# Performance work log

Hardware: AMD Instinct MI355X
Metric: run time of the kernel (lower is better)

Reference implementation:

```python
import jax, jax.numpy as jnp
import numpy as np

DIM = 96          # adapter bottleneck dim
K = 3             # conv kernel size

def quick_gelu(x):
    return x * jax.nn.sigmoid(1.702 * x)

def setup_inputs() -> dict:
    key = jax.random.key(0)
    ks = jax.random.split(key, 12)
    B, H, W, C = 64, 28, 28, 384
    x   = jax.random.normal(ks[0], (B, H, W, C), jnp.float32)
    # adapter down/up (xavier-ish scale for down; up is zero-init in the
    # original but we use small random so gradients flow in tests)
    Wd  = jax.random.normal(ks[1], (C, DIM), jnp.float32) * 0.05
    bd  = jnp.zeros((DIM,), jnp.float32)
    Wu  = jax.random.normal(ks[2], (DIM, C), jnp.float32) * 0.02
    bu  = jnp.zeros((C,), jnp.float32)
    # meta_net: Linear(C,64) -> ReLU -> Linear(64,64)
    Wm1 = jax.random.normal(ks[3], (C, 64), jnp.float32) * 0.05
    bm1 = jnp.zeros((64,), jnp.float32)
    Wm2 = jax.random.normal(ks[4], (64, 64), jnp.float32) * 0.1
    bm2 = jnp.zeros((64,), jnp.float32)
    # conv hypernet: Linear(64, DIM*DIM*K*K)
    Wh  = jax.random.normal(ks[5], (64, DIM * DIM * K * K), jnp.float32) * 0.01
    bh  = jnp.zeros((DIM * DIM * K * K,), jnp.float32)
    # learned layer embedding
    emb = jax.random.normal(ks[6], (64,), jnp.float32)
    return {"x": x, "Wd": Wd, "bd": bd, "Wm1": Wm1, "bm1": bm1,
            "Wm2": Wm2, "bm2": bm2, "Wh": Wh, "bh": bh, "emb": emb,
            "Wu": Wu, "bu": bu}

def reference(x, Wd, bd, Wm1, bm1, Wm2, bm2, Wh, bh, emb, Wu, bu):
    B, H, W, C = x.shape
    # meta_net(x) then mean over spatial dims -> per-sample prompt feature [B,64]
    h = jax.nn.relu(jnp.einsum('bhwc,cd->bhwd', x, Wm1) + bm1)
    prompt = jnp.mean(jnp.einsum('bhwd,de->bhwe', h, Wm2) + bm2, axis=(1, 2))  # [B,64]
    # hypernet: per-sample dynamic conv weights (fuse_type='add')
    wflat = (emb[None, :] + prompt) @ Wh + bh                 # [B, DIM*DIM*9]
    wconv = wflat.reshape(B * DIM, DIM, K, K)                 # grouped OIHW
    # adapter down + QuickGELU
    xd = quick_gelu(jnp.einsum('bhwc,cd->bhwd', x, Wd) + bd)  # [B,H,W,DIM]
    # fused batched dynamic conv via grouped conv (groups = B)
    xg = xd.transpose(0, 3, 1, 2).reshape(1, B * DIM, H, W)   # [1,B*DIM,H,W]
    yg = jax.lax.conv_general_dilated(
        xg, wconv, window_strides=(1, 1), padding=((1, 1), (1, 1)),
        dimension_numbers=('NCHW', 'OIHW', 'NCHW'), feature_group_count=B)
    y = yg.reshape(B, DIM, H, W).transpose(0, 2, 3, 1)        # [B,H,W,DIM]
    y = quick_gelu(y)  # dropout is identity in eval mode
    return jnp.einsum('bhwd,dc->bhwc', y, Wu) + bu
```

## Files before the change

kernel.cpp:

```cpp
#include <hip/hip_runtime.h>
#include <hip/hip_fp16.h>

#define BATCH 64
#define HH    28
#define WW2   28
#define HWPX  784
#define PTOT  50176
#define CIN   384
#define DIM   96
#define MDIM  64
#define JTOT  82944
#define WSAMP 82944

#define XD_OFF 0u
#define Y_OFF  9633792u
#define WP_OFF 19267584u
#define HS_OFF 29884416u
#define Z_OFF  29900800u
#define WUT_OFF 29917184u

typedef _Float16 f16x8 __attribute__((ext_vector_type(8)));
typedef _Float16 f16x4 __attribute__((ext_vector_type(4)));
typedef float f32x4 __attribute__((ext_vector_type(4)));

__device__ __forceinline__ float qgelu(float v) {
    return v / (1.f + __expf(-1.702f * v));
}

__global__ void k0_wcvt(const float* __restrict__ Wm1,
                        const float* __restrict__ Wd,
                        const float* __restrict__ Wu,
                        _Float16* __restrict__ Wt,
                        _Float16* __restrict__ WuT)
{
    int i = blockIdx.x * 256 + threadIdx.x;
    if (i < 61440) {
        int o = i / CIN, k = i - o * CIN;
        float v = (o < MDIM) ? Wm1[k * MDIM + o] : Wd[k * DIM + (o - MDIM)];
        Wt[i] = (_Float16)v;
    } else {
        int j = i - 61440;
        int c = j / DIM, d = j - c * DIM;
        WuT[j] = (_Float16)Wu[d * CIN + c];
    }
}

__global__ __launch_bounds__(512, 4) void k1_mfma(
    const float* __restrict__ x, const _Float16* __restrict__ Wt,
    const float* __restrict__ bm1, const float* __restrict__ bd,
    float* __restrict__ hsum, __half* __restrict__ xd)
{
    __shared__ char smem[25088];
    _Float16* xds = (_Float16*)smem;
    float*   hred = (float*)(smem + 24576);

    const int t = threadIdx.x;
    const int p0 = blockIdx.x * 128;
    const int lane = t & 63, w = t >> 6;
    const int wm = w >> 1, wn = w & 1;
    const int rl = lane & 15, q = lane >> 4;

    const float* a0 = x + (size_t)(p0 + wm * 32 + rl) * CIN + q * 8;
    const float* a1 = a0 + 16 * CIN;
    const _Float16* bp0 = Wt + (wn * 80 + rl) * CIN + q * 8;

    f32x4 acc[2][5];
    #pragma unroll
    for (int mf = 0; mf < 2; ++mf)
        #pragma unroll
        for (int nf = 0; nf < 5; ++nf) acc[mf][nf] = (f32x4){0.f, 0.f, 0.f, 0.f};

    #pragma unroll
    for (int kc = 0; kc < 12; ++kc) {
        f16x8 bv[5];
        #pragma unroll
        for (int nf = 0; nf < 5; ++nf)
            bv[nf] = *(const f16x8*)(bp0 + nf * 16 * CIN + kc * 32);

        float4 fa0 = *(const float4*)(a0 + kc * 32);
        float4 fa1 = *(const float4*)(a0 + kc * 32 + 4);
        float4 fb0 = *(const float4*)(a1 + kc * 32);
        float4 fb1 = *(const float4*)(a1 + kc * 32 + 4);

        f16x8 av[2];
        av[0][0] = (_Float16)fa0.x; av[0][1] = (_Float16)fa0.y;
        av[0][2] = (_Float16)fa0.z; av[0][3] = (_Float16)fa0.w;
        av[0][4] = (_Float16)fa1.x; av[0][5] = (_Float16)fa1.y;
        av[0][6] = (_Float16)fa1.z; av[0][7] = (_Float16)fa1.w;
        av[1][0] = (_Float16)fb0.x; av[1][1] = (_Float16)fb0.y;
        av[1][2] = (_Float16)fb0.z; av[1][3] = (_Float16)fb0.w;
        av[1][4] = (_Float16)fb1.x; av[1][5] = (_Float16)fb1.y;
        av[1][6] = (_Float16)fb1.z; av[1][7] = (_Float16)fb1.w;

        #pragma unroll
        for (int mf = 0; mf < 2; ++mf)
            #pragma unroll
            for (int nf = 0; nf < 5; ++nf)
                acc[mf][nf] = __builtin_amdgcn_mfma_f32_16x16x32_f16(
                    av[mf], bv[nf], acc[mf][nf], 0, 0, 0);
    }

    if (t < 128) hred[t] = 0.f;
    __syncthreads();

    const int s0 = p0 / HWPX, s_last = (p0 + 127) / HWPX;
    #pragma unroll
    for (int mf = 0; mf < 2; ++mf) {
        #pragma unroll
        for (int nf = 0; nf < 5; ++nf) {
            const int col = wn * 80 + nf * 16 + rl;
            #pragma unroll
            for (int j = 0; j < 4; ++j) {
                const int rr = wm * 32 + mf * 16 + q * 4 + j;
                float v = acc[mf][nf][j];
                if (col < 64) {
                    v = fmaxf(v + bm1[col], 0.f);
                    int sloc = (p0 + rr) / HWPX - s0;
                    atomicAdd(&hred[sloc * 64 + col], v);
                } else {
                    int e = col - 64;
                    xds[rr * 96 + e] = (_Float16)qgelu(v + bd[e]);
                }
            }
        }
    }
    __syncthreads();

    if (t < 128) {
        int sloc = t >> 6, col = t & 63, s = s0 + sloc;
        if (s <= s_last) atomicAdd(&hsum[s * 64 + col], hred[t]);
    }
    #pragma unroll
    for (int i = 0; i < 3; ++i) {
        int e = t + i * 512;
        *(uint4*)((__half*)xd + (size_t)p0 * 96 + e * 8) = *(uint4*)(xds + e * 8);
    }
}

__global__ void k2a_prompt(const float* __restrict__ hsum,
                           const float* __restrict__ Wm2,
                           const float* __restrict__ bm2,
                           const float* __restrict__ emb,
                           float* __restrict__ z)
{
    int idx = blockIdx.x * 256 + threadIdx.x;
    int b = idx >> 6, m = idx & 63;
    float acc = 0.f;
    #pragma unroll 8
    for (int d = 0; d < 64; ++d) acc += hsum[b * 64 + d] * Wm2[d * 64 + m];
    z[idx] = emb[m] + acc * (1.f / 784.f) + bm2[m];
}

__global__ __launch_bounds__(256) void k2b_hyper(
    const float* __restrict__ z, const float* __restrict__ Wh,
    const float* __restrict__ bh, __half* __restrict__ wperm)
{
    __shared__ float zs[4096];
    const int t = threadIdx.x;
    for (int idx = t; idx < 4096; idx += 256) zs[idx] = z[idx];
    const int j = blockIdx.x * 256 + t;
    float wh[64];
    #pragma unroll 8
    for (int m = 0; m < 64; ++m) wh[m] = Wh[(size_t)m * JTOT + j];
    __syncthreads();

    const int o = j / 864, rem = j % 864;
    const int i = rem / 9, t9 = rem % 9;
    const int base = o * 864 + t9 * 96 + i;
    const float bj = bh[j];
    for (int b = 0; b < 64; ++b) {
        float a = bj;
        const float4* zz = (const float4*)(zs + b * 64);
        #pragma unroll
        for (int m4 = 0; m4 < 16; ++m4) {
            float4 v = zz[m4];
            a += v.x * wh[4 * m4] + v.y * wh[4 * m4 + 1] +
                 v.z * wh[4 * m4 + 2] + v.w * wh[4 * m4 + 3];
        }
        wperm[(size_t)b * WSAMP + base] = __float2half(a);
    }
}

__global__ __launch_bounds__(256) void k3_mfma(
    const __half* __restrict__ xd, const __half* __restrict__ wperm,
    __half* __restrict__ y)
{
    __shared__ __half sm[17600];
    const int t = threadIdx.x;

    const int n = blockIdx.x;
    const int xcd = n & 7, jj0 = n >> 3;
    const int b = xcd * 8 + jj0 / 7;
    const int rt = jj0 % 7;
    const int h0 = rt * 4;

    if (t < 16) *(uint4*)(sm + 17472 + t * 8) = uint4{0u, 0u, 0u, 0u};
    for (int idx = t; idx < 2016; idx += 256) {
        int pix = idx / 12, q = idx - pix * 12;
        int r = pix / 28, col = pix - r * 28;
        int g = h0 - 1 + r;
        uint4 v = {0u, 0u, 0u, 0u};
        if ((unsigned)g < 28u)
            v = *(const uint4*)(xd + (size_t)(b * HWPX + g * 28 + col) * 96 + q * 8);
        *(uint4*)(sm + pix * 104 + q * 8) = v;
    }
    __syncthreads();

    const int lane = t & 63, w = t >> 6;
    const int wm = w >> 1, wn = w & 1;
    const int mloc = lane & 15, klo = (lane >> 4) * 8;
    const int base_m = wm * 64;

    int oh_[4], ow_[4]; bool pv[4];
    #pragma unroll
    for (int mf = 0; mf < 4; ++mf) {
        int p = base_m + mf * 16 + mloc;
        pv[mf] = (p < 112);
        int pp = pv[mf] ? p : 0;
        oh_[mf] = pp / 28; ow_[mf] = pp - oh_[mf] * 28;
    }
    const __half* wp = wperm + (size_t)b * WSAMP + (wn * 48 + mloc) * 864 + klo;

    f32x4 acc[4][3];
    #pragma unroll
    for (int mf = 0; mf < 4; ++mf)
        #pragma unroll
        for (int nf = 0; nf < 3; ++nf) acc[mf][nf] = (f32x4){0.f, 0.f, 0.f, 0.f};

    #pragma unroll
    for (int kh = 0; kh < 3; ++kh) {
        #pragma unroll
        for (int kw = 0; kw < 3; ++kw) {
            const int t9 = kh * 3 + kw;
            int abase[4];
            #pragma unroll
            for (int mf = 0; mf < 4; ++mf) {
                int iw = ow_[mf] + kw - 1;
                bool valid = pv[mf] && ((unsigned)iw < 28u);
                abase[mf] = valid ? ((oh_[mf] + kh) * 28 + iw) * 104 + klo
                                  : 17472 + klo;
            }
            #pragma unroll
            for (int ic = 0; ic < 3; ++ic) {
                f16x8 av[4], bv[3];
                #pragma unroll
                for (int nf = 0; nf < 3; ++nf)
                    bv[nf] = *(const f16x8*)(wp + nf * 13824 + t9 * 96 + ic * 32);
                #pragma unroll
                for (int mf = 0; mf < 4; ++mf)
                    av[mf] = *(const f16x8*)(sm + abase[mf] + ic * 32);
                #pragma unroll
                for (int mf = 0; mf < 4; ++mf)
                    #pragma unroll
                    for (int nf = 0; nf < 3; ++nf)
                        acc[mf][nf] = __builtin_amdgcn_mfma_f32_16x16x32_f16(
                            av[mf], bv[nf], acc[mf][nf], 0, 0, 0);
            }
        }
    }
    __syncthreads();

    #pragma unroll
    for (int mf = 0; mf < 4; ++mf) {
        #pragma unroll
        for (int nf = 0; nf < 3; ++nf) {
            const int o = wn * 48 + nf * 16 + mloc;
            #pragma unroll
            for (int j = 0; j < 4; ++j) {
                int p = base_m + mf * 16 + (lane >> 4) * 4 + j;
                if (p < 112)
                    sm[p * 104 + o] = __float2half(qgelu(acc[mf][nf][j]));
            }
        }
    }
    __syncthreads();
    for (int idx = t; idx < 1344; idx += 256) {
        int pix = idx / 12, q = idx - pix * 12;
        *(uint4*)(y + (size_t)(b * HWPX + h0 * 28 + pix) * 96 + q * 8) =
            *(uint4*)(sm + pix * 104 + q * 8);
    }
}

__global__ __launch_bounds__(512, 2) void k4_mfma(
    const __half* __restrict__ y, const _Float16* __restrict__ WuT,
    const float* __restrict__ bu, float* __restrict__ out)
{
    __shared__ __half ys[128 * 104];
    const int t = threadIdx.x;
    const int p0 = blockIdx.x * 128;

    #pragma unroll
    for (int i = 0; i < 3; ++i) {
        int idx = t + i * 512;
        int pix = idx / 12, q = idx - pix * 12;
        *(uint4*)(ys + pix * 104 + q * 8) =
            *(const uint4*)(y + (size_t)(p0 + pix) * 96 + q * 8);
    }

    const int lane = t & 63, w = t >> 6;
    const int wm = w >> 2, wn = w & 3;
    const int mloc = lane & 15, klo = (lane >> 4) * 8;

    float bcol[6];
    #pragma unroll
    for (int nf = 0; nf < 6; ++nf) bcol[nf] = bu[wn * 96 + nf * 16 + mloc];
    __syncthreads();

    f32x4 acc[4][6];
    #pragma unroll
    for (int mf = 0; mf < 4; ++mf)
        #pragma unroll
        for (int nf = 0; nf < 6; ++nf) acc[mf][nf] = (f32x4){0.f, 0.f, 0.f, 0.f};

    #pragma unroll
    for (int kc = 0; kc < 3; ++kc) {
        f16x8 av[4], bv[6];
        #pragma unroll
        for (int nf = 0; nf < 6; ++nf)
            bv[nf] = *(const f16x8*)(WuT + (wn * 96 + nf * 16 + mloc) * 96 + kc * 32 + klo);
        #pragma unroll
        for (int mf = 0; mf < 4; ++mf)
            av[mf] = *(const f16x8*)(ys + (wm * 64 + mf * 16 + mloc) * 104 + kc * 32 + klo);
        #pragma unroll
        for (int mf = 0; mf < 4; ++mf)
            #pragma unroll
            for (int nf = 0; nf < 6; ++nf)
                acc[mf][nf] = __builtin_amdgcn_mfma_f32_16x16x32_f16(
                    av[mf], bv[nf], acc[mf][nf], 0, 0, 0);
    }

    #pragma unroll
    for (int mf = 0; mf < 4; ++mf) {
        #pragma unroll
        for (int nf = 0; nf < 6; ++nf) {
            const int c = wn * 96 + nf * 16 + mloc;
            #pragma unroll
            for (int j = 0; j < 4; ++j) {
                int p = p0 + wm * 64 + mf * 16 + (lane >> 4) * 4 + j;
                out[(size_t)p * CIN + c] = acc[mf][nf][j] + bcol[nf];
            }
        }
    }
}

extern "C" void kernel_launch(void* const* d_in, const int* in_sizes, int n_in,
                              void* d_out, int out_size, void* d_ws, size_t ws_size,
                              hipStream_t stream)
{
    const float* x   = (const float*)d_in[0];
    const float* Wd  = (const float*)d_in[1];
    const float* bd  = (const float*)d_in[2];
    const float* Wm1 = (const float*)d_in[3];
    const float* bm1 = (const float*)d_in[4];
    const float* Wm2 = (const float*)d_in[5];
    const float* bm2 = (const float*)d_in[6];
    const float* Wh  = (const float*)d_in[7];
    const float* bh  = (const float*)d_in[8];
    const float* emb = (const float*)d_in[9];
    const float* Wu  = (const float*)d_in[10];
    const float* bu  = (const float*)d_in[11];
    float* out = (float*)d_out;

    char* ws = (char*)d_ws;
    __half*   xd    = (__half*)(ws + XD_OFF);
    __half*   ybuf  = (__half*)(ws + Y_OFF);
    __half*   wperm = (__half*)(ws + WP_OFF);
    float*    hsum  = (float*)(ws + HS_OFF);
    float*    z     = (float*)(ws + Z_OFF);
    _Float16* Wt    = (_Float16*)(ws + WP_OFF);
    _Float16* WuT   = (_Float16*)(ws + WUT_OFF);

    hipMemsetAsync(hsum, 0, 64 * 64 * sizeof(float), stream);

    k0_wcvt<<<384, 256, 0, stream>>>(Wm1, Wd, Wu, Wt, WuT);
    k1_mfma<<<392, 512, 0, stream>>>(x, Wt, bm1, bd, hsum, xd);
    k2a_prompt<<<16, 256, 0, stream>>>(hsum, Wm2, bm2, emb, z);
    k2b_hyper<<<324, 256, 0, stream>>>(z, Wh, bh, wperm);
    k3_mfma<<<448, 256, 0, stream>>>(xd, wperm, ybuf);
    k4_mfma<<<392, 512, 0, stream>>>(ybuf, WuT, bu, out);
}
```

Measured before the change: 167.9 us.

## Stage k1 GEMM tiles through LDS with register prefetch and halve block rows

```diff
diff --git a/kernel.cpp b/kernel.cpp
--- a/kernel.cpp
+++ b/kernel.cpp
@@ -45,82 +45,96 @@
     }
 }
 
-__global__ __launch_bounds__(512, 4) void k1_mfma(
+__global__ __launch_bounds__(512, 6) void k1_mfma(
     const float* __restrict__ x, const _Float16* __restrict__ Wt,
     const float* __restrict__ bm1, const float* __restrict__ bd,
     float* __restrict__ hsum, __half* __restrict__ xd)
 {
-    __shared__ char smem[25088];
+    __shared__ char smem[18432];
+    _Float16* As  = (_Float16*)smem;
+    _Float16* Bs  = (_Float16*)(smem + 5120);
+    float*   hred = (float*)(smem + 17920);
     _Float16* xds = (_Float16*)smem;
-    float*   hred = (float*)(smem + 24576);
 
     const int t = threadIdx.x;
-    const int p0 = blockIdx.x * 128;
+    const int p0 = blockIdx.x * 64;
     const int lane = t & 63, w = t >> 6;
     const int wm = w >> 1, wn = w & 1;
     const int rl = lane & 15, q = lane >> 4;
 
-    const float* a0 = x + (size_t)(p0 + wm * 32 + rl) * CIN + q * 8;
-    const float* a1 = a0 + 16 * CIN;
-    const _Float16* bp0 = Wt + (wn * 80 + rl) * CIN + q * 8;
-
-    f32x4 acc[2][5];
-    #pragma unroll
-    for (int mf = 0; mf < 2; ++mf)
-        #pragma unroll
-        for (int nf = 0; nf < 5; ++nf) acc[mf][nf] = (f32x4){0.f, 0.f, 0.f, 0.f};
+    const int arow = t >> 3, aq = t & 7;
+    const int brow = t >> 2, bq = t & 3;
+
+    const float*    ag  = x + (size_t)(p0 + arow) * CIN + aq * 4;
+    const _Float16* bg0 = Wt + brow * CIN + bq * 8;
+    const _Float16* bg1 = Wt + (brow + 128) * CIN + bq * 8;
+
+    float4 ra;
+    uint4  rb0, rb1;
+
+#define LOADC(kc_) do {                                           \
+    ra  = *(const float4*)(ag + (kc_) * 32);                      \
+    rb0 = *(const uint4*)(bg0 + (kc_) * 32);                      \
+    if (t < 128) rb1 = *(const uint4*)(bg1 + (kc_) * 32);         \
+} while (0)
+
+#define WRITEC() do {                                             \
+    f16x4 h;                                                      \
+    h[0] = (_Float16)ra.x; h[1] = (_Float16)ra.y;                 \
+    h[2] = (_Float16)ra.z; h[3] = (_Float16)ra.w;                 \
+    *(f16x4*)(As + arow * 40 + aq * 4) = h;                       \
+    *(uint4*)(Bs + brow * 40 + bq * 8) = rb0;                     \
+    if (t < 128)                                                  \
+        *(uint4*)(Bs + (brow + 128) * 40 + bq * 8) = rb1;         \
+} while (0)
+
+    f32x4 acc[5];
+    #pragma unroll
+    for (int nf = 0; nf < 5; ++nf) acc[nf] = (f32x4){0.f, 0.f, 0.f, 0.f};
+
+    LOADC(0);
 
     #pragma unroll
     for (int kc = 0; kc < 12; ++kc) {
-        f16x8 bv[5];
+        WRITEC();
+        __syncthreads();
+
+        if (kc + 1 < 12) LOADC(kc + 1);
+
+        f16x8 av, bv[5];
+        av = *(f16x8*)(As + (wm * 16 + rl) * 40 + q * 8);
         #pragma unroll
         for (int nf = 0; nf < 5; ++nf)
-            bv[nf] = *(const f16x8*)(bp0 + nf * 16 * CIN + kc * 32);
-
-        float4 fa0 = *(const float4*)(a0 + kc * 32);
-        float4 fa1 = *(const float4*)(a0 + kc * 32 + 4);
-        float4 fb0 = *(const float4*)(a1 + kc * 32);
-        float4 fb1 = *(const float4*)(a1 + kc * 32 + 4);
-
-        f16x8 av[2];
-        av[0][0] = (_Float16)fa0.x; av[0][1] = (_Float16)fa0.y;
-        av[0][2] = (_Float16)fa0.z; av[0][3] = (_Float16)fa0.w;
-        av[0][4] = (_Float16)fa1.x; av[0][5] = (_Float16)fa1.y;
-        av[0][6] = (_Float16)fa1.z; av[0][7] = (_Float16)fa1.w;
-        av[1][0] = (_Float16)fb0.x; av[1][1] = (_Float16)fb0.y;
-        av[1][2] = (_Float16)fb0.z; av[1][3] = (_Float16)fb0.w;
-        av[1][4] = (_Float16)fb1.x; av[1][5] = (_Float16)fb1.y;
-        av[1][6] = (_Float16)fb1.z; av[1][7] = (_Float16)fb1.w;
-
-        #pragma unroll
-        for (int mf = 0; mf < 2; ++mf)
-            #pragma unroll
-            for (int nf = 0; nf < 5; ++nf)
-                acc[mf][nf] = __builtin_amdgcn_mfma_f32_16x16x32_f16(
-                    av[mf], bv[nf], acc[mf][nf], 0, 0, 0);
-    }
+            bv[nf] = *(f16x8*)(Bs + (wn * 80 + nf * 16 + rl) * 40 + q * 8);
+
+        #pragma unroll
+        for (int nf = 0; nf < 5; ++nf)
+            acc[nf] = __builtin_amdgcn_mfma_f32_16x16x32_f16(
+                av, bv[nf], acc[nf], 0, 0, 0);
+
+        __syncthreads();
+    }
+#undef LOADC
+#undef WRITEC
 
     if (t < 128) hred[t] = 0.f;
     __syncthreads();
 
-    const int s0 = p0 / HWPX, s_last = (p0 + 127) / HWPX;
-    #pragma unroll
-    for (int mf = 0; mf < 2; ++mf) {
-        #pragma unroll
-        for (int nf = 0; nf < 5; ++nf) {
-            const int col = wn * 80 + nf * 16 + rl;
-            #pragma unroll
-            for (int j = 0; j < 4; ++j) {
-                const int rr = wm * 32 + mf * 16 + q * 4 + j;
-                float v = acc[mf][nf][j];
-                if (col < 64) {
-                    v = fmaxf(v + bm1[col], 0.f);
-                    int sloc = (p0 + rr) / HWPX - s0;
-                    atomicAdd(&hred[sloc * 64 + col], v);
-                } else {
-                    int e = col - 64;
-                    xds[rr * 96 + e] = (_Float16)qgelu(v + bd[e]);
-                }
+    const int s0 = p0 / HWPX, s_last = (p0 + 63) / HWPX;
+    #pragma unroll
+    for (int nf = 0; nf < 5; ++nf) {
+        const int col = wn * 80 + nf * 16 + rl;
+        #pragma unroll
+        for (int j = 0; j < 4; ++j) {
+            const int rr = wm * 16 + q * 4 + j;
+            float v = acc[nf][j];
+            if (col < 64) {
+                v = fmaxf(v + bm1[col], 0.f);
+                int sloc = (p0 + rr) / HWPX - s0;
+                atomicAdd(&hred[sloc * 64 + col], v);
+            } else {
+                int e = col - 64;
+                xds[rr * 96 + e] = (_Float16)qgelu(v + bd[e]);
             }
         }
     }
@@ -130,10 +144,11 @@
         int sloc = t >> 6, col = t & 63, s = s0 + sloc;
         if (s <= s_last) atomicAdd(&hsum[s * 64 + col], hred[t]);
     }
-    #pragma unroll
-    for (int i = 0; i < 3; ++i) {
-        int e = t + i * 512;
-        *(uint4*)((__half*)xd + (size_t)p0 * 96 + e * 8) = *(uint4*)(xds + e * 8);
+    {
+        *(uint4*)((__half*)xd + (size_t)p0 * 96 + t * 8) = *(uint4*)(xds + t * 8);
+        if (t < 256)
+            *(uint4*)((__half*)xd + (size_t)p0 * 96 + (t + 512) * 8) =
+                *(uint4*)(xds + (t + 512) * 8);
     }
 }
 
@@ -373,7 +388,7 @@
     hipMemsetAsync(hsum, 0, 64 * 64 * sizeof(float), stream);
 
     k0_wcvt<<<384, 256, 0, stream>>>(Wm1, Wd, Wu, Wt, WuT);
-    k1_mfma<<<392, 512, 0, stream>>>(x, Wt, bm1, bd, hsum, xd);
+    k1_mfma<<<784, 512, 0, stream>>>(x, Wt, bm1, bd, hsum, xd);
     k2a_prompt<<<16, 256, 0, stream>>>(hsum, Wm2, bm2, emb, z);
     k2b_hyper<<<324, 256, 0, stream>>>(z, Wh, bh, wperm);
     k3_mfma<<<448, 256, 0, stream>>>(xd, wperm, ybuf);
```

Measured after the change: 141.1 us. 1.19x faster.
